# Optimization experiments

Hardware: AMD Instinct MI355X
Metric: run time of the kernel (lower is better)

## Reference

```python
import jax, jax.numpy as jnp
import numpy as np

B, N, D, C = 2, 65536, 128, 128          # batch, n_entries, input_dim, channel_dim
DEG, N_ACTIVE, STRIDE = 16, 4096, 16     # ring-neighbor sparse structure


def _build_indices():
    """Replicates the original module's Python intersection loops exactly,
    flattening them into (src_i, src_j, pair_out) gather/scatter index arrays.
    k[:, e, :] = sum_m a[:, i_th[m], :] * b[:, j_th[m], :] for each write slot e.
    Each slot e is written exactly once, so scatter-add == the original set."""
    neigh = [[] for _ in range(N)]
    for t in range(N_ACTIVE):
        i = t * STRIDE
        neigh[i] = [((t + dlt) % N_ACTIVE) * STRIDE for dlt in range(1, DEG + 1)]
    src_i, src_j, out = [], [], []
    e = 0
    for i in range(N):
        if not neigh[i]:
            continue
        i_element = list(neigh[i]) + [i]
        i_set = set(i_element)
        for j in neigh[i]:
            j_list = neigh[j]
            j_set = set(j_list)
            j_th = [m for m in j_list if m in i_set]      # order of j's list
            i_th = [m for m in i_element if m in j_set]   # order of i_element
            for ai, bi in zip(i_th, j_th):
                src_i.append(ai)
                src_j.append(bi)
                out.append(e)
            e += 1
    return (np.asarray(src_i, np.int32), np.asarray(src_j, np.int32),
            np.asarray(out, np.int32))


def setup_inputs() -> dict:
    key = jax.random.key(0)
    ks = jax.random.split(key, 8)
    s = 1.0 / np.sqrt(D)
    src_i, src_j, pair_out = _build_indices()
    return {
        "x": jax.random.normal(ks[0], (B, N, D), jnp.float32),
        "ln_in_w": jnp.ones((D,), jnp.float32),
        "ln_in_b": jnp.zeros((D,), jnp.float32),
        "Wla": jax.random.normal(ks[1], (C, D), jnp.float32) * s,
        "bla": jnp.zeros((C,), jnp.float32),
        "Wga": jax.random.normal(ks[2], (C, D), jnp.float32) * s,
        "bga": jnp.zeros((C,), jnp.float32),
        "Wlb": jax.random.normal(ks[3], (C, D), jnp.float32) * s,
        "blb": jnp.zeros((C,), jnp.float32),
        "Wgb": jax.random.normal(ks[4], (C, D), jnp.float32) * s,
        "bgb": jnp.zeros((C,), jnp.float32),
        "ln_o_w": jnp.ones((C,), jnp.float32),
        "ln_o_b": jnp.zeros((C,), jnp.float32),
        "Wgo": jax.random.normal(ks[5], (D, D), jnp.float32) * s,
        "bgo": jnp.zeros((D,), jnp.float32),
        "Wlo": jax.random.normal(ks[6], (D, C), jnp.float32) * s,
        "blo": jnp.zeros((D,), jnp.float32),
        "src_i": jnp.asarray(src_i),
        "src_j": jnp.asarray(src_j),
        "pair_out": jnp.asarray(pair_out),
    }


def _layernorm(x, w, b, eps=1e-5):
    mu = jnp.mean(x, axis=-1, keepdims=True)
    var = jnp.mean(jnp.square(x - mu), axis=-1, keepdims=True)
    return (x - mu) * jax.lax.rsqrt(var + eps) * w + b


def reference(x, ln_in_w, ln_in_b, Wla, bla, Wga, bga, Wlb, blb, Wgb, bgb,
              ln_o_w, ln_o_b, Wgo, bgo, Wlo, blo, src_i, src_j, pair_out):
    xn = _layernorm(x, ln_in_w, ln_in_b)                              # [B,N,D]
    a = jax.nn.sigmoid(xn @ Wga.T + bga) * (xn @ Wla.T + bla)         # [B,N,C]
    b = jax.nn.sigmoid(xn @ Wgb.T + bgb) * (xn @ Wlb.T + blb)         # [B,N,C]
    # triangular update: gather-multiply-sum-scatter over precomputed pairs
    prod = a[:, src_i, :] * b[:, src_j, :]                            # [B,P,C]
    k = jnp.zeros_like(a).at[:, pair_out, :].add(prod)                # [B,N,C]
    out = jax.nn.sigmoid(xn @ Wgo.T + bgo) * (_layernorm(k, ln_o_w, ln_o_b) @ Wlo.T + blo)
    return out
```

## Files before the change

kernel.cpp:

```cpp
#include <hip/hip_runtime.h>


#define BB 2
#define NN 65536
#define DD 128
#define CC 128
#define NA 4096
#define STR 16
#define WSZ 16384

typedef short short8v __attribute__((ext_vector_type(8)));
typedef __bf16 bf16x8 __attribute__((ext_vector_type(8)));
typedef float f32x4 __attribute__((ext_vector_type(4)));
typedef float f32x2 __attribute__((ext_vector_type(2)));

__device__ __forceinline__ float sigf(float v) { return 1.0f / (1.0f + __expf(-v)); }
__device__ __forceinline__ short nbf(float f) {
    union { __bf16 h; short s; } u; u.h = (__bf16)f; return u.s;
}
__device__ __forceinline__ bf16x8 s2b(short8v s) {
    union { short8v s; bf16x8 b; } u; u.s = s; return u.b;
}

__global__ __launch_bounds__(256)
void kern_wcvt(const float* __restrict__ Wla, const float* __restrict__ Wga,
               const float* __restrict__ Wlb, const float* __restrict__ Wgb,
               const float* __restrict__ Wgo, const float* __restrict__ Wlo,
               const float* __restrict__ lnw, const float* __restrict__ lnb,
               const float* __restrict__ lnow, const float* __restrict__ lnob,
               const float* __restrict__ bla, const float* __restrict__ bga,
               const float* __restrict__ blb, const float* __restrict__ bgb,
               const float* __restrict__ bgo, const float* __restrict__ blo,
               short* __restrict__ wbf, float* __restrict__ vtab)
{
    const int b = blockIdx.x;
    if (b < 64) {
        const int i  = b * 256 + threadIdx.x;
        const int ch = i >> 7, d = i & 127;
        const int pos = ((ch >> 4) * 4 + (d >> 5)) * 512
                      + ((((d >> 3) & 3) * 16 + (ch & 15)) * 8) + (d & 7);
        const float wi = lnw[d], wo = lnow[d];
        wbf[pos]           = nbf(Wla[i] * wi);
        wbf[WSZ + pos]     = nbf(Wga[i] * wi);
        wbf[2 * WSZ + pos] = nbf(Wlb[i] * wi);
        wbf[3 * WSZ + pos] = nbf(Wgb[i] * wi);
        wbf[4 * WSZ + pos] = nbf(Wgo[i] * wi);
        wbf[5 * WSZ + pos] = nbf(Wlo[i] * wo);
    } else {
        const int t = (b - 64) * 256 + threadIdx.x;
        const int m = t >> 7, c = t & 127;
        const float* Wr = (m == 0) ? Wla : (m == 1) ? Wga : (m == 2) ? Wlb
                        : (m == 3) ? Wgb : (m == 4) ? Wgo : Wlo;
        const float* bb = (m == 5) ? lnob : lnb;
        const float* bi = (m == 0) ? bla : (m == 1) ? bga : (m == 2) ? blb
                        : (m == 3) ? bgb : (m == 4) ? bgo : blo;
        const float* row = Wr + (size_t)c * DD;
        float acc = 0.f;
        for (int d = 0; d < DD; d += 4) {
            const f32x4 w4 = *(const f32x4*)(row + d);
            const f32x4 b4 = *(const f32x4*)(bb + d);
            acc += w4[0]*b4[0] + w4[1]*b4[1] + w4[2]*b4[2] + w4[3]*b4[3];
        }
        vtab[m * 128 + c] = acc + bi[c];
    }
}

__global__ __launch_bounds__(64)
void kern_ab(const float* __restrict__ x, const short* __restrict__ wbf,
             const float* __restrict__ vtab, float* __restrict__ cbuf)
{
    const int l     = threadIdx.x;
    const int bid   = blockIdx.x;
    const int batch = bid >> 9;
    const int t0    = ((bid & 511) >> 1) << 4;
    const int nt0   = (bid & 1) * 4;
    const int lr    = l & 15;
    const int q     = l >> 4;
    const int fl    = l * 8;

    const float* xr = x + ((size_t)batch * NN + (size_t)(t0 + lr) * STR) * DD + q * 8;
    f32x4 v[4][2];
    #pragma unroll
    for (int kk = 0; kk < 4; ++kk) {
        v[kk][0] = *(const f32x4*)(xr + kk * 32);
        v[kk][1] = *(const f32x4*)(xr + kk * 32 + 4);
    }
    float s = 0.f, ss = 0.f;
    #pragma unroll
    for (int kk = 0; kk < 4; ++kk)
        #pragma unroll
        for (int h = 0; h < 2; ++h)
            #pragma unroll
            for (int j = 0; j < 4; ++j) { const float f = v[kk][h][j]; s += f; ss += f * f; }
    s += __shfl_xor(s, 16); ss += __shfl_xor(ss, 16);
    s += __shfl_xor(s, 32); ss += __shfl_xor(ss, 32);
    const float mu = s * (1.0f / 128.0f);
    const float rs = rsqrtf(ss * (1.0f / 128.0f) - mu * mu + 1e-5f);
    const float p  = -mu * rs;

    bf16x8 af[4];
    #pragma unroll
    for (int kk = 0; kk < 4; ++kk) {
        short8v t;
        #pragma unroll
        for (int j = 0; j < 4; ++j) {
            t[j]     = nbf(v[kk][0][j] * rs + p);
            t[4 + j] = nbf(v[kk][1][j] * rs + p);
        }
        af[kk] = s2b(t);
    }

    const short* wla = wbf;
    const short* wga = wbf + WSZ;
    const short* wlb = wbf + 2 * WSZ;
    const short* wgb = wbf + 3 * WSZ;

    #pragma unroll
    for (int nt = 0; nt < 4; ++nt) {
        const int col  = (nt0 + nt) * 16 + lr;
        const int base = ((nt0 + nt) * 4) * 512 + fl;
        f32x4 ala = {0.f,0.f,0.f,0.f}, aga = {0.f,0.f,0.f,0.f};
        f32x4 alb = {0.f,0.f,0.f,0.f}, agb = {0.f,0.f,0.f,0.f};
        #pragma unroll
        for (int kk = 0; kk < 4; ++kk) {
            const int o = base + kk * 512;
            ala = __builtin_amdgcn_mfma_f32_16x16x32_bf16(af[kk], *(const bf16x8*)(wla + o), ala, 0, 0, 0);
            aga = __builtin_amdgcn_mfma_f32_16x16x32_bf16(af[kk], *(const bf16x8*)(wga + o), aga, 0, 0, 0);
            alb = __builtin_amdgcn_mfma_f32_16x16x32_bf16(af[kk], *(const bf16x8*)(wlb + o), alb, 0, 0, 0);
            agb = __builtin_amdgcn_mfma_f32_16x16x32_bf16(af[kk], *(const bf16x8*)(wgb + o), agb, 0, 0, 0);
        }
        const float vla = vtab[col], vga = vtab[128 + col];
        const float vlb = vtab[256 + col], vgb = vtab[384 + col];
        #pragma unroll
        for (int r = 0; r < 4; ++r) {
            const float av = sigf(aga[r] + vga) * (ala[r] + vla);
            const float bv = sigf(agb[r] + vgb) * (alb[r] + vlb);
            cbuf[((size_t)batch * NA + t0 + q * 4 + r) * CC + col] = av * bv;
        }
    }
}

__global__ __launch_bounds__(64)
void kern_out(const float* __restrict__ x, const short* __restrict__ wbf,
              const float* __restrict__ vtab, const float* __restrict__ cbuf,
              float* __restrict__ out)
{
    __shared__ float kls[16][132];
    const int bid   = blockIdx.x;
    const int swz   = (bid & 7) * 1024 + (bid >> 3);
    const int batch = swz >> 12;
    const int t     = swz & 4095;
    const int row0  = t * 16;

    const int l  = threadIdx.x;
    const int lr = l & 15, lk = l >> 4;
    const int fl = l * 8;

    const float* xr = x + ((size_t)batch * NN + row0 + lr) * DD + lk * 8;
    f32x4 v[4][2];
    #pragma unroll
    for (int kk = 0; kk < 4; ++kk) {
        v[kk][0] = *(const f32x4*)(xr + kk * 32);
        v[kk][1] = *(const f32x4*)(xr + kk * 32 + 4);
    }

    const int c2 = l * 2;
    f32x2 cv[15];
    #pragma unroll
    for (int sx = 14; sx >= 0; --sx)
        cv[sx] = *(const f32x2*)(cbuf + ((size_t)batch * NA + ((t + sx + 2) & (NA - 1))) * CC + c2);

    {
        f32x2 z = {0.f, 0.f};
        *(f32x2*)&kls[15][c2] = z;
        float s0 = 0.f, s1 = 0.f;
        #pragma unroll
        for (int sx = 14; sx >= 0; --sx) {
            s0 += cv[sx][0]; s1 += cv[sx][1];
            f32x2 o = {s0, s1};
            *(f32x2*)&kls[sx][c2] = o;
        }
    }

    bf16x8 afx[4];
    {
        float s = 0.f, ss = 0.f;
        #pragma unroll
        for (int kk = 0; kk < 4; ++kk)
            #pragma unroll
            for (int h = 0; h < 2; ++h)
                #pragma unroll
                for (int j = 0; j < 4; ++j) { const float f = v[kk][h][j]; s += f; ss += f * f; }
        s += __shfl_xor(s, 16); ss += __shfl_xor(ss, 16);
        s += __shfl_xor(s, 32); ss += __shfl_xor(ss, 32);
        const float mu = s * (1.0f / 128.0f);
        const float rs = rsqrtf(ss * (1.0f / 128.0f) - mu * mu + 1e-5f);
        const float p  = -mu * rs;
        #pragma unroll
        for (int kk = 0; kk < 4; ++kk) {
            short8v o;
            #pragma unroll
            for (int j = 0; j < 4; ++j) {
                o[j]     = nbf(v[kk][0][j] * rs + p);
                o[4 + j] = nbf(v[kk][1][j] * rs + p);
            }
            afx[kk] = s2b(o);
        }
    }

    bf16x8 afk[4];
    {
        f32x4 kr[4][2];
        #pragma unroll
        for (int kk = 0; kk < 4; ++kk) {
            kr[kk][0] = *(const f32x4*)&kls[lr][kk * 32 + lk * 8];
            kr[kk][1] = *(const f32x4*)&kls[lr][kk * 32 + lk * 8 + 4];
        }
        float ks = 0.f, kss = 0.f;
        #pragma unroll
        for (int kk = 0; kk < 4; ++kk)
            #pragma unroll
            for (int h = 0; h < 2; ++h)
                #pragma unroll
                for (int j = 0; j < 4; ++j) { const float f = kr[kk][h][j]; ks += f; kss += f * f; }
        ks += __shfl_xor(ks, 16); kss += __shfl_xor(kss, 16);
        ks += __shfl_xor(ks, 32); kss += __shfl_xor(kss, 32);
        const float kmu = ks * (1.0f / 128.0f);
        const float krs = rsqrtf(kss * (1.0f / 128.0f) - kmu * kmu + 1e-5f);
        const float kp  = -kmu * krs;
        #pragma unroll
        for (int kk = 0; kk < 4; ++kk) {
            short8v o;
            #pragma unroll
            for (int j = 0; j < 4; ++j) {
                o[j]     = nbf(kr[kk][0][j] * krs + kp);
                o[4 + j] = nbf(kr[kk][1][j] * krs + kp);
            }
            afk[kk] = s2b(o);
        }
    }

    const short* wgo = wbf + 4 * WSZ;
    const short* wlo = wbf + 5 * WSZ;
    const float* vgo = vtab + 4 * 128;
    const float* vlo = vtab + 5 * 128;
    #pragma unroll
    for (int nt = 0; nt < 8; ++nt) {
        f32x4 ag = {0.f,0.f,0.f,0.f}, ah = {0.f,0.f,0.f,0.f};
        #pragma unroll
        for (int kk = 0; kk < 4; ++kk) {
            const int o = (nt * 4 + kk) * 512 + fl;
            ag = __builtin_amdgcn_mfma_f32_16x16x32_bf16(afx[kk], *(const bf16x8*)(wgo + o), ag, 0, 0, 0);
            ah = __builtin_amdgcn_mfma_f32_16x16x32_bf16(afk[kk], *(const bf16x8*)(wlo + o), ah, 0, 0, 0);
        }
        const int   col = nt * 16 + lr;
        const float vg  = vgo[col];
        const float vl  = vlo[col];
        #pragma unroll
        for (int r = 0; r < 4; ++r) {
            const size_t rowa = (size_t)batch * NN + row0 + lk * 4 + r;
            out[rowa * DD + col] = sigf(ag[r] + vg) * (ah[r] + vl);
        }
    }
}

extern "C" void kernel_launch(void* const* d_in, const int* in_sizes, int n_in,
                              void* d_out, int out_size, void* d_ws, size_t ws_size,
                              hipStream_t stream)
{
    const float* x    = (const float*)d_in[0];
    const float* lnw  = (const float*)d_in[1];
    const float* lnb  = (const float*)d_in[2];
    const float* Wla  = (const float*)d_in[3];
    const float* bla  = (const float*)d_in[4];
    const float* Wga  = (const float*)d_in[5];
    const float* bga  = (const float*)d_in[6];
    const float* Wlb  = (const float*)d_in[7];
    const float* blb  = (const float*)d_in[8];
    const float* Wgb  = (const float*)d_in[9];
    const float* bgb  = (const float*)d_in[10];
    const float* lnow = (const float*)d_in[11];
    const float* lnob = (const float*)d_in[12];
    const float* Wgo  = (const float*)d_in[13];
    const float* bgo  = (const float*)d_in[14];
    const float* Wlo  = (const float*)d_in[15];
    const float* blo  = (const float*)d_in[16];

    float* cbuf = (float*)d_ws;
    short* wbf  = (short*)((char*)d_ws + (size_t)BB * NA * CC * 4);
    float* vtab = (float*)((char*)wbf + 6 * WSZ * sizeof(short));
    float* out  = (float*)d_out;

    hipLaunchKernelGGL(kern_wcvt, dim3(67), dim3(256), 0, stream,
                       Wla, Wga, Wlb, Wgb, Wgo, Wlo,
                       lnw, lnb, lnow, lnob,
                       bla, bga, blb, bgb, bgo, blo, wbf, vtab);
    hipLaunchKernelGGL(kern_ab, dim3(BB * 512), dim3(64), 0, stream,
                       x, wbf, vtab, cbuf);
    hipLaunchKernelGGL(kern_out, dim3(BB * 4096), dim3(64), 0, stream,
                       x, wbf, vtab, cbuf, out);
}
```

Baseline: 52.21 us.

## Pack four waves per block and store prefix sums in fp16 LDS

Both compute kernels now launch 256-thread blocks holding four independent waves instead of one 64-thread block per wave, with block and wave indices remapped. Fewer, larger blocks cut dispatch overhead and raise residency. The kern_out prefix-sum staging buffer is stored as packed fp16 instead of fp32, halving LDS footprint and read traffic. This adds fp16 rounding of the k values before the layernorm, so accuracy may drop slightly.

```diff
diff --git a/kernel.cpp b/kernel.cpp
--- a/kernel.cpp
+++ b/kernel.cpp
@@ -11,6 +11,9 @@
 
 typedef short short8v __attribute__((ext_vector_type(8)));
 typedef __bf16 bf16x8 __attribute__((ext_vector_type(8)));
+typedef _Float16 f16x2 __attribute__((ext_vector_type(2)));
+typedef _Float16 f16x8 __attribute__((ext_vector_type(8)));
+typedef __fp16 fp16x2 __attribute__((ext_vector_type(2)));
 typedef float f32x4 __attribute__((ext_vector_type(4)));
 typedef float f32x2 __attribute__((ext_vector_type(2)));
 
@@ -20,6 +23,9 @@
 }
 __device__ __forceinline__ bf16x8 s2b(short8v s) {
     union { short8v s; bf16x8 b; } u; u.s = s; return u.b;
+}
+__device__ __forceinline__ f16x2 pkh(float a, float b) {
+    union { fp16x2 p; f16x2 f; } u; u.p = __builtin_amdgcn_cvt_pkrtz(a, b); return u.f;
 }
 
 __global__ __launch_bounds__(256)
@@ -65,12 +71,13 @@
     }
 }
 
-__global__ __launch_bounds__(64)
+__global__ __launch_bounds__(256)
 void kern_ab(const float* __restrict__ x, const short* __restrict__ wbf,
              const float* __restrict__ vtab, float* __restrict__ cbuf)
 {
-    const int l     = threadIdx.x;
-    const int bid   = blockIdx.x;
+    const int wv    = threadIdx.x >> 6;
+    const int l     = threadIdx.x & 63;
+    const int bid   = blockIdx.x * 4 + wv;
     const int batch = bid >> 9;
     const int t0    = ((bid & 511) >> 1) << 4;
     const int nt0   = (bid & 1) * 4;
@@ -140,19 +147,21 @@
     }
 }
 
-__global__ __launch_bounds__(64)
+__global__ __launch_bounds__(256)
 void kern_out(const float* __restrict__ x, const short* __restrict__ wbf,
               const float* __restrict__ vtab, const float* __restrict__ cbuf,
               float* __restrict__ out)
 {
-    __shared__ float kls[16][132];
-    const int bid   = blockIdx.x;
-    const int swz   = (bid & 7) * 1024 + (bid >> 3);
-    const int batch = swz >> 12;
-    const int t     = swz & 4095;
+    __shared__ _Float16 kls[4][16][136];
+    const int bid = blockIdx.x;
+    const int swz = (bid & 7) * 256 + (bid >> 3);
+    const int wv  = threadIdx.x >> 6;
+    const int l   = threadIdx.x & 63;
+    const int gw  = swz * 4 + wv;
+    const int batch = gw >> 12;
+    const int t     = gw & 4095;
     const int row0  = t * 16;
 
-    const int l  = threadIdx.x;
     const int lr = l & 15, lk = l >> 4;
     const int fl = l * 8;
 
@@ -171,14 +180,13 @@
         cv[sx] = *(const f32x2*)(cbuf + ((size_t)batch * NA + ((t + sx + 2) & (NA - 1))) * CC + c2);
 
     {
-        f32x2 z = {0.f, 0.f};
-        *(f32x2*)&kls[15][c2] = z;
+        f16x2 z = {(_Float16)0.f, (_Float16)0.f};
+        *(f16x2*)&kls[wv][15][c2] = z;
         float s0 = 0.f, s1 = 0.f;
         #pragma unroll
         for (int sx = 14; sx >= 0; --sx) {
             s0 += cv[sx][0]; s1 += cv[sx][1];
-            f32x2 o = {s0, s1};
-            *(f32x2*)&kls[sx][c2] = o;
+            *(f16x2*)&kls[wv][sx][c2] = pkh(s0, s1);
         }
     }
 
@@ -210,19 +218,15 @@
 
     bf16x8 afk[4];
     {
-        f32x4 kr[4][2];
-        #pragma unroll
-        for (int kk = 0; kk < 4; ++kk) {
-            kr[kk][0] = *(const f32x4*)&kls[lr][kk * 32 + lk * 8];
-            kr[kk][1] = *(const f32x4*)&kls[lr][kk * 32 + lk * 8 + 4];
-        }
+        f16x8 kraw[4];
+        #pragma unroll
+        for (int kk = 0; kk < 4; ++kk)
+            kraw[kk] = *(const f16x8*)&kls[wv][lr][kk * 32 + lk * 8];
         float ks = 0.f, kss = 0.f;
         #pragma unroll
         for (int kk = 0; kk < 4; ++kk)
             #pragma unroll
-            for (int h = 0; h < 2; ++h)
-                #pragma unroll
-                for (int j = 0; j < 4; ++j) { const float f = kr[kk][h][j]; ks += f; kss += f * f; }
+            for (int j = 0; j < 8; ++j) { const float f = (float)kraw[kk][j]; ks += f; kss += f * f; }
         ks += __shfl_xor(ks, 16); kss += __shfl_xor(kss, 16);
         ks += __shfl_xor(ks, 32); kss += __shfl_xor(kss, 32);
         const float kmu = ks * (1.0f / 128.0f);
@@ -232,10 +236,8 @@
         for (int kk = 0; kk < 4; ++kk) {
             short8v o;
             #pragma unroll
-            for (int j = 0; j < 4; ++j) {
-                o[j]     = nbf(kr[kk][0][j] * krs + kp);
-                o[4 + j] = nbf(kr[kk][1][j] * krs + kp);
-            }
+            for (int j = 0; j < 8; ++j)
+                o[j] = nbf((float)kraw[kk][j] * krs + kp);
             afk[kk] = s2b(o);
         }
     }
@@ -295,8 +297,8 @@
                        Wla, Wga, Wlb, Wgb, Wgo, Wlo,
                        lnw, lnb, lnow, lnob,
                        bla, bga, blb, bgb, bgo, blo, wbf, vtab);
-    hipLaunchKernelGGL(kern_ab, dim3(BB * 512), dim3(64), 0, stream,
+    hipLaunchKernelGGL(kern_ab, dim3(BB * 128), dim3(256), 0, stream,
                        x, wbf, vtab, cbuf);
-    hipLaunchKernelGGL(kern_out, dim3(BB * 4096), dim3(64), 0, stream,
+    hipLaunchKernelGGL(kern_out, dim3(BB * 1024), dim3(256), 0, stream,
                        x, wbf, vtab, cbuf, out);
 }
```

After: 53.26 us. 1.02x slower.
